# Kernel optimization log

Hardware: AMD Instinct MI355X
Metric: run time of the kernel (lower is better)

Reference implementation:

```python
import jax, jax.numpy as jnp
import numpy as np

BLOCK_K = 32   # BLOCK_K_SIZE_MIN in the original Triton kernel
BLOCK_N = 32   # output-block granularity of the hash


def _hash_indices(random_numbers, num_nb, num_kb, num_red_kb):
    # universal hash of (n_block, k_block) -> reduced k-block index
    r = random_numbers.astype(jnp.uint32)
    nb = jnp.arange(num_nb, dtype=jnp.uint32)[:, None]
    kb = jnp.arange(num_kb, dtype=jnp.uint32)[None, :]
    hv = (kb * r[0] + nb * r[1] + r[2]) ^ r[3]
    return (hv % jnp.uint32(num_red_kb)).astype(jnp.int32)  # [num_nb, num_kb]


def _ssl_forward(x, weight, bias, random_numbers):
    orig_shape = x.shape
    K = orig_shape[-1]
    x2 = x.reshape(-1, K)                       # [M, K]
    N, red_K = weight.shape
    num_kb = K // BLOCK_K
    num_red_kb = red_K // BLOCK_K
    num_nb = N // BLOCK_N
    h = _hash_indices(random_numbers, num_nb, num_kb, num_red_kb)  # [num_nb, num_kb]
    # Gather the virtual full weight from the reduced weight via hash indices.
    wb = weight.reshape(num_nb, BLOCK_N, num_red_kb, BLOCK_K)
    w_full = jnp.take_along_axis(wb, h[:, None, :, None], axis=2)  # [num_nb, BN, num_kb, BK]
    w_full = w_full.reshape(N, K)
    y = x2 @ w_full.T
    if bias is not None:
        y = y + bias
    return y.reshape(*orig_shape[:-1], N)


def setup_inputs() -> dict:
    key = jax.random.key(0)
    k1, k2, k3 = jax.random.split(key, 3)
    in_features, out_features, redn_factor, seed = 8192, 512, 8, 1024
    red_in = ((in_features // redn_factor + BLOCK_K - 1) // BLOCK_K) * BLOCK_K  # 1024
    x = jax.random.normal(k1, (4, 2048, in_features), dtype=jnp.float32)
    bound = 1.0 / np.sqrt(red_in)
    weight = jax.random.uniform(k2, (out_features, red_in), jnp.float32, -bound, bound)
    bias = jax.random.uniform(k3, (out_features,), jnp.float32, -bound, bound)
    rng = np.random.default_rng(seed)
    random_numbers = jnp.asarray(rng.integers(1, 2**31 - 1, size=4), dtype=jnp.int32)
    return {"x": x, "weight": weight, "bias": bias,
            "random_numbers": random_numbers, "redn_factor": redn_factor}


def reference(x, weight, bias, random_numbers, redn_factor):
    return _ssl_forward(x, weight, bias, random_numbers)
```

## Files before the change

### kernel.cpp

```cpp
#include <hip/hip_runtime.h>
#include <hip/hip_bf16.h>
#include <stdint.h>


typedef __bf16 bf16x4_t __attribute__((ext_vector_type(4)));
typedef __bf16 bf16x8_t __attribute__((ext_vector_type(8)));
typedef float f32x4 __attribute__((ext_vector_type(4)));

#define BM 128
#define BN 128
#define BK 32
#define LDSK 40
#define KSPLIT 4

__global__ void init_out(float* __restrict__ Out, const float* __restrict__ Bias,
                         int N, int total4) {
  int i = blockIdx.x * blockDim.x + threadIdx.x;
  if (i < total4) {
    int idx = i << 2;
    int n = idx % N;
    *(f32x4*)(Out + idx) = *(const f32x4*)(Bias + n);
  }
}

__device__ __forceinline__ void wg_barrier_lds() {
  __builtin_amdgcn_sched_barrier(0);
  asm volatile("s_waitcnt lgkmcnt(0)" ::: "memory");
  __builtin_amdgcn_s_barrier();
  __builtin_amdgcn_sched_barrier(0);
}

__global__ __launch_bounds__(256, 1) void ssl_gemm(
    const float* __restrict__ X,
    const float* __restrict__ W,
    const int* __restrict__ RN,
    float* __restrict__ Out,
    int M, int N, int K, int redK, uint32_t numRedKb, int mTiles, int nTiles) {
  __shared__ __align__(16) __bf16 As[BM * LDSK];
  __shared__ __align__(16) __bf16 Bs[BN * LDSK];

  const uint32_t r0 = (uint32_t)RN[0], r1 = (uint32_t)RN[1];
  const uint32_t r2 = (uint32_t)RN[2], r3 = (uint32_t)RN[3];
  const uint32_t redMask = numRedKb - 1u;
  const bool pow2 = (numRedKb & (numRedKb - 1u)) == 0u;

  const int id = blockIdx.x;
  const int mTile = id % mTiles;
  const int rest = id / mTiles;
  const int nTile = rest % nTiles;
  const int kChunk = rest / nTiles;

  const int tid = threadIdx.x;
  const int wave = tid >> 6;
  const int lane = tid & 63;
  const int wm = wave >> 1, wn = wave & 1;

  const int lRow = tid >> 3;
  const int lCol = (tid & 7) << 2;
  const float* aBase = X + (size_t)(mTile * BM + lRow) * K + lCol;
  const float* bBase = W + (size_t)(nTile * BN + lRow) * redK + lCol;

  auto loadA = [&](int kb, f32x4* r) {
    const float* p = aBase + (size_t)kb * BK;
#pragma unroll
    for (int i = 0; i < 4; ++i)
      r[i] = *(const f32x4*)(p + (size_t)(i * 32) * K);
  };
  auto loadB = [&](int kb, f32x4* r) {
    const uint32_t kk = (uint32_t)kb * r0 + r2;
#pragma unroll
    for (int i = 0; i < 4; ++i) {
      const uint32_t nb = (uint32_t)(nTile * (BN / 32) + i);
      const uint32_t hv = (kk + nb * r1) ^ r3;
      const uint32_t h = pow2 ? (hv & redMask) : (hv % numRedKb);
      r[i] = *(const f32x4*)(bBase + (size_t)(i * 32) * redK + h * 32u);
    }
  };
  auto stage = [&](const f32x4* rA, const f32x4* rB) {
#pragma unroll
    for (int i = 0; i < 4; ++i) {
      bf16x4_t a, b;
#pragma unroll
      for (int j = 0; j < 4; ++j) {
        a[j] = (__bf16)rA[i][j];
        b[j] = (__bf16)rB[i][j];
      }
      *(bf16x4_t*)&As[(i * 32 + lRow) * LDSK + lCol] = a;
      *(bf16x4_t*)&Bs[(i * 32 + lRow) * LDSK + lCol] = b;
    }
  };

  f32x4 acc[4][4] = {};
  auto compute = [&]() {
    bf16x8_t af[4], bfr[4];
    const int kOff = (lane >> 4) << 3;
    const int r16 = lane & 15;
#pragma unroll
    for (int mi = 0; mi < 4; ++mi)
      af[mi] = *(const bf16x8_t*)&As[((wm << 6) + (mi << 4) + r16) * LDSK + kOff];
#pragma unroll
    for (int ni = 0; ni < 4; ++ni)
      bfr[ni] = *(const bf16x8_t*)&Bs[((wn << 6) + (ni << 4) + r16) * LDSK + kOff];
#pragma unroll
    for (int mi = 0; mi < 4; ++mi)
#pragma unroll
      for (int ni = 0; ni < 4; ++ni)
        acc[mi][ni] = __builtin_amdgcn_mfma_f32_16x16x32_bf16(
            af[mi], bfr[ni], acc[mi][ni], 0, 0, 0);
  };

  const int numKb = K / BK;
  const int kbN = numKb / KSPLIT;
  const int kb0 = kChunk * kbN;
  f32x4 a0[4], b0[4], a1[4], b1[4];
  loadA(kb0, a0);
  loadB(kb0, b0);
  for (int i = 0; i < kbN; i += 2) {
    if (i + 1 < kbN) { loadA(kb0 + i + 1, a1); loadB(kb0 + i + 1, b1); }
    wg_barrier_lds();
    stage(a0, b0);
    wg_barrier_lds();
    compute();
    if (i + 2 < kbN) { loadA(kb0 + i + 2, a0); loadB(kb0 + i + 2, b0); }
    wg_barrier_lds();
    stage(a1, b1);
    wg_barrier_lds();
    compute();
  }

  const int mBase = mTile * BM + (wm << 6);
  const int nBase = nTile * BN + (wn << 6);
#pragma unroll
  for (int ni = 0; ni < 4; ++ni) {
    const int n = nBase + (ni << 4) + (lane & 15);
#pragma unroll
    for (int mi = 0; mi < 4; ++mi) {
      const int m0 = mBase + (mi << 4) + ((lane >> 4) << 2);
#pragma unroll
      for (int r = 0; r < 4; ++r)
        unsafeAtomicAdd(&Out[(size_t)(m0 + r) * N + n], acc[mi][ni][r]);
    }
  }
}

extern "C" void kernel_launch(void* const* d_in, const int* in_sizes, int n_in,
                              void* d_out, int out_size, void* d_ws, size_t ws_size,
                              hipStream_t stream) {
  const float* X = (const float*)d_in[0];
  const float* W = (const float*)d_in[1];
  const float* Bias = (const float*)d_in[2];
  const int* RN = (const int*)d_in[3];
  float* Out = (float*)d_out;

  const int N = in_sizes[2];
  const int M = out_size / N;
  const int K = in_sizes[0] / M;
  const int redK = in_sizes[1] / N;
  const uint32_t numRedKb = (uint32_t)(redK / 32);

  const int total4 = out_size / 4;
  init_out<<<(total4 + 255) / 256, 256, 0, stream>>>(Out, Bias, N, total4);

  const int mTiles = M / BM;
  const int nTiles = N / BN;
  dim3 grid(mTiles * nTiles * KSPLIT), block(256);
  ssl_gemm<<<grid, block, 0, stream>>>(X, W, RN, Out,
                                       M, N, K, redK, numRedKb, mTiles, nTiles);
}
```

Before: 499.7 us.

## Load weight fragments straight to registers, dropping B shared-memory staging

Each wave now loads its own weight-tile fragment directly from global memory in MFMA operand layout and converts it to bf16 in registers, so the B tile no longer goes through shared memory. This halves LDS use and LDS traffic per k-step, and the launch bound is raised to 3 blocks per CU for more occupancy. The main loop is simplified to single-buffering with one k-block in flight. The cost is redundant global reads of W across the two waves sharing a column half, less latency hiding than the old two-stage loop, and register pressure under the tighter launch bound.

```diff
diff --git a/kernel.cpp b/kernel.cpp
--- a/kernel.cpp
+++ b/kernel.cpp
@@ -30,14 +30,13 @@
   __builtin_amdgcn_sched_barrier(0);
 }
 
-__global__ __launch_bounds__(256, 1) void ssl_gemm(
+__global__ __launch_bounds__(256, 3) void ssl_gemm(
     const float* __restrict__ X,
     const float* __restrict__ W,
     const int* __restrict__ RN,
     float* __restrict__ Out,
     int M, int N, int K, int redK, uint32_t numRedKb, int mTiles, int nTiles) {
   __shared__ __align__(16) __bf16 As[BM * LDSK];
-  __shared__ __align__(16) __bf16 Bs[BN * LDSK];
 
   const uint32_t r0 = (uint32_t)RN[0], r1 = (uint32_t)RN[1];
   const uint32_t r2 = (uint32_t)RN[2], r3 = (uint32_t)RN[3];
@@ -58,7 +57,10 @@
   const int lRow = tid >> 3;
   const int lCol = (tid & 7) << 2;
   const float* aBase = X + (size_t)(mTile * BM + lRow) * K + lCol;
-  const float* bBase = W + (size_t)(nTile * BN + lRow) * redK + lCol;
+
+  const int r16 = lane & 15;
+  const int e0 = (lane >> 4) << 3;
+  const float* wBase = W + (size_t)(nTile * BN + wn * 64 + r16) * redK + e0;
 
   auto loadA = [&](int kb, f32x4* r) {
     const float* p = aBase + (size_t)kb * BK;
@@ -66,66 +68,69 @@
     for (int i = 0; i < 4; ++i)
       r[i] = *(const f32x4*)(p + (size_t)(i * 32) * K);
   };
-  auto loadB = [&](int kb, f32x4* r) {
+
+  f32x4 bF[8];
+  auto loadBf = [&](int kb) {
     const uint32_t kk = (uint32_t)kb * r0 + r2;
 #pragma unroll
-    for (int i = 0; i < 4; ++i) {
-      const uint32_t nb = (uint32_t)(nTile * (BN / 32) + i);
+    for (int ni = 0; ni < 4; ++ni) {
+      const uint32_t nb = (uint32_t)(nTile * (BN / 32) + wn * 2 + (ni >> 1));
       const uint32_t hv = (kk + nb * r1) ^ r3;
       const uint32_t h = pow2 ? (hv & redMask) : (hv % numRedKb);
-      r[i] = *(const f32x4*)(bBase + (size_t)(i * 32) * redK + h * 32u);
+      const float* p = wBase + (size_t)(ni * 16) * redK + h * 32u;
+      bF[2 * ni]     = *(const f32x4*)(p);
+      bF[2 * ni + 1] = *(const f32x4*)(p + 4);
     }
   };
-  auto stage = [&](const f32x4* rA, const f32x4* rB) {
+
+  auto stage = [&](const f32x4* rA) {
 #pragma unroll
     for (int i = 0; i < 4; ++i) {
-      bf16x4_t a, b;
+      bf16x4_t v;
 #pragma unroll
-      for (int j = 0; j < 4; ++j) {
-        a[j] = (__bf16)rA[i][j];
-        b[j] = (__bf16)rB[i][j];
-      }
-      *(bf16x4_t*)&As[(i * 32 + lRow) * LDSK + lCol] = a;
-      *(bf16x4_t*)&Bs[(i * 32 + lRow) * LDSK + lCol] = b;
+      for (int j = 0; j < 4; ++j) v[j] = (__bf16)rA[i][j];
+      *(bf16x4_t*)&As[(i * 32 + lRow) * LDSK + lCol] = v;
     }
   };
 
   f32x4 acc[4][4] = {};
-  auto compute = [&]() {
-    bf16x8_t af[4], bfr[4];
-    const int kOff = (lane >> 4) << 3;
-    const int r16 = lane & 15;
+
+  const int numKb = K / BK;
+  const int kbN = numKb / KSPLIT;
+  const int kb0 = kChunk * kbN;
+
+  f32x4 a[4];
+  loadA(kb0, a);
+  loadBf(kb0);
+  for (int i = 0; i < kbN; ++i) {
+    wg_barrier_lds();
+    stage(a);
+    if (i + 1 < kbN) loadA(kb0 + i + 1, a);
+    wg_barrier_lds();
+
+    bf16x8_t bb[4];
+#pragma unroll
+    for (int ni = 0; ni < 4; ++ni) {
+      bf16x8_t t;
+#pragma unroll
+      for (int j = 0; j < 4; ++j) {
+        t[j]     = (__bf16)bF[2 * ni][j];
+        t[4 + j] = (__bf16)bF[2 * ni + 1][j];
+      }
+      bb[ni] = t;
+    }
+    if (i + 1 < kbN) loadBf(kb0 + i + 1);
+
+    bf16x8_t af[4];
 #pragma unroll
     for (int mi = 0; mi < 4; ++mi)
-      af[mi] = *(const bf16x8_t*)&As[((wm << 6) + (mi << 4) + r16) * LDSK + kOff];
-#pragma unroll
-    for (int ni = 0; ni < 4; ++ni)
-      bfr[ni] = *(const bf16x8_t*)&Bs[((wn << 6) + (ni << 4) + r16) * LDSK + kOff];
+      af[mi] = *(const bf16x8_t*)&As[((wm << 6) + (mi << 4) + r16) * LDSK + e0];
 #pragma unroll
     for (int mi = 0; mi < 4; ++mi)
 #pragma unroll
       for (int ni = 0; ni < 4; ++ni)
         acc[mi][ni] = __builtin_amdgcn_mfma_f32_16x16x32_bf16(
-            af[mi], bfr[ni], acc[mi][ni], 0, 0, 0);
-  };
-
-  const int numKb = K / BK;
-  const int kbN = numKb / KSPLIT;
-  const int kb0 = kChunk * kbN;
-  f32x4 a0[4], b0[4], a1[4], b1[4];
-  loadA(kb0, a0);
-  loadB(kb0, b0);
-  for (int i = 0; i < kbN; i += 2) {
-    if (i + 1 < kbN) { loadA(kb0 + i + 1, a1); loadB(kb0 + i + 1, b1); }
-    wg_barrier_lds();
-    stage(a0, b0);
-    wg_barrier_lds();
-    compute();
-    if (i + 2 < kbN) { loadA(kb0 + i + 2, a0); loadB(kb0 + i + 2, b0); }
-    wg_barrier_lds();
-    stage(a1, b1);
-    wg_barrier_lds();
-    compute();
+            af[mi], bb[ni], acc[mi][ni], 0, 0, 0);
   }
 
   const int mBase = mTile * BM + (wm << 6);
```

Measured after the change: 652.3 us. 1.31x slower.
